# Kernel optimization log

Measured on AMD Instinct MI355X. Metric: run time of the kernel, lower is better.

## Reference

```python
import jax, jax.numpy as jnp
import numpy as np

B, S, H = 4, 1024, 1024
NH = 16
D = H // NH  # attention_head_size = 64
L = 9        # num_labels
MAXREL = 5
B_PERSON = 1
I_PERSON = 2
LN_EPS = 1e-5


def setup_inputs() -> dict:
    key = jax.random.key(0)
    ks = jax.random.split(key, 16)
    lin = lambda k, i, o: 0.02 * jax.random.normal(k, (i, o), jnp.float32)
    return {
        "sequence_output": jax.random.normal(ks[0], (B, S, H), jnp.float32),
        "Wq": lin(ks[1], H, H), "bq": jnp.zeros((H,), jnp.float32),
        "Wk": lin(ks[2], H, H), "bk": jnp.zeros((H,), jnp.float32),
        "Wv": lin(ks[3], H, H), "bv": jnp.zeros((H,), jnp.float32),
        "Wo": lin(ks[4], H, H), "bo": jnp.zeros((H,), jnp.float32),
        "ln_g": jnp.ones((H,), jnp.float32), "ln_b": jnp.zeros((H,), jnp.float32),
        "Ws": lin(ks[5], H, L), "bs": jnp.zeros((L,), jnp.float32),
        "entity_bias": 0.1 * jax.random.normal(ks[6], (L,), jnp.float32),
        "rel_pos_emb": jax.random.normal(ks[7], (2 * MAXREL + 1, D), jnp.float32),  # declared but unused in forward math, matching the torch module
    }


def reference(sequence_output, Wq, bq, Wk, bk, Wv, bv, Wo, bo, ln_g, ln_b, Ws, bs, entity_bias, rel_pos_emb):
    x = sequence_output  # [B,S,H]
    b, s, _ = x.shape

    def heads(t):  # [B,S,H] -> [B,NH,S,D]
        return t.reshape(b, s, NH, D).transpose(0, 2, 1, 3)

    q = heads(x @ Wq + bq)
    k = heads(x @ Wk + bk)
    v = heads(x @ Wv + bv)

    scores = jnp.einsum('bhqd,bhkd->bhqk', q, k)  # [B,NH,S,S]

    r = jnp.arange(s, dtype=jnp.float32)
    dist = jnp.abs(r[:, None] - r[None, :])                 # |i-j|, [S,S]
    pos_bias = jnp.exp(-0.1 * jnp.clip(dist, 0.0, float(MAXREL)))
    # torch order: (scores + pos_bias) / sqrt(D) + distance_mask
    scores = (scores + pos_bias) / np.sqrt(D) + (-0.1) * dist

    probs = jax.nn.softmax(scores, axis=-1)  # dropout is identity in eval
    ctx = jnp.einsum('bhqk,bhkd->bhqd', probs, v)
    ctx = ctx.transpose(0, 2, 1, 3).reshape(b, s, H)

    y = x + (ctx @ Wo + bo)  # residual
    mu = y.mean(-1, keepdims=True)
    var = y.var(-1, keepdims=True)
    yn = (y - mu) / jnp.sqrt(var + LN_EPS) * ln_g + ln_b

    span_logits = yn @ Ws + bs  # [B,S,L]
    # entity-bias loop: if argmax(span_logits[i,j-1]) == B-PERSON, add entity_bias[I-PERSON] twice to final[i,j,I-PERSON]
    prev_is_b = (jnp.argmax(span_logits[:, :-1, :], axis=-1) == B_PERSON).astype(span_logits.dtype)  # [B,S-1]
    final_logits = span_logits.at[:, 1:, I_PERSON].add(2.0 * entity_bias[I_PERSON] * prev_is_b)
    return final_logits
```

## Files before the change

### kernel.cpp

```cpp
#include <hip/hip_runtime.h>
#include <hip/hip_bf16.h>
#include <math.h>

typedef unsigned short ush;
typedef __attribute__((ext_vector_type(8))) _Float16 fragh;
typedef __attribute__((ext_vector_type(4))) _Float16 half4;
typedef __attribute__((ext_vector_type(4))) float f32x4;

#define S_   1024
#define H_   1024
#define NH_  16
#define D_   64
#define L_   9
#define MB_  (1048576ull)

__device__ __forceinline__ void load_lds16(const ush* g, const ush* l) {
  __builtin_amdgcn_global_load_lds(
      (const __attribute__((address_space(1))) void*)g,
      (__attribute__((address_space(3))) void*)l, 16, 0, 0);
}

__global__ __launch_bounds__(256) void prep(
    const float* __restrict__ x,
    const float* W0, const float* W1, const float* W2, const float* W3,
    const float* __restrict__ Ws,
    ush* __restrict__ xh, ush* T0, ush* T1, ush* T2, ush* T3,
    float* __restrict__ WsT) {
  __shared__ __align__(16) float Ls[64][68];
  const int bid = blockIdx.x;
  const int tid = threadIdx.x;

  if (bid < 2048) {
    const size_t i = ((size_t)bid * 256 + tid) * 8;
    float4 a = *(const float4*)&x[i];
    float4 b = *(const float4*)&x[i + 4];
    fragh v;
    v[0] = (_Float16)a.x; v[1] = (_Float16)a.y;
    v[2] = (_Float16)a.z; v[3] = (_Float16)a.w;
    v[4] = (_Float16)b.x; v[5] = (_Float16)b.y;
    v[6] = (_Float16)b.z; v[7] = (_Float16)b.w;
    *(fragh*)&xh[i] = v;
    return;
  }
  if (bid >= 3072) {
    for (int idx = tid; idx < 1024 * 9; idx += 256) {
      const int r = idx / 9, c = idx - r * 9;
      WsT[c * 1024 + r] = Ws[idx];
    }
    return;
  }
  const int flat = bid - 2048;
  const int wz = flat >> 8, wy = (flat >> 4) & 15, wx = flat & 15;
  const float* W = (wz == 0) ? W0 : (wz == 1) ? W1 : (wz == 2) ? W2 : W3;
  ush* Th = (wz == 0) ? T0 : (wz == 1) ? T1 : (wz == 2) ? T2 : T3;
  const int n0 = wx * 64, k0 = wy * 64;
#pragma unroll
  for (int it = 0; it < 4; it++) {
    int f = tid + 256 * it;
    int row = f >> 4, nc = (f & 15) * 4;
    *(float4*)&Ls[row][nc] = *(const float4*)&W[(size_t)(k0 + row) * 1024 + n0 + nc];
  }
  __syncthreads();
#pragma unroll
  for (int it = 0; it < 2; it++) {
    int f = tid + 256 * it;
    int nrow = f >> 3, kc = (f & 7) * 8;
    fragh v;
#pragma unroll
    for (int u = 0; u < 8; u++) v[u] = (_Float16)Ls[kc + u][nrow];
    *(fragh*)&Th[(size_t)(n0 + nrow) * 1024 + k0 + kc] = v;
  }
}

__global__ __launch_bounds__(256) void gemm_qkv(
    const ush* __restrict__ xh,
    const ush* __restrict__ Bq, const ush* __restrict__ Bk,
    const ush* __restrict__ Bv,
    const float* __restrict__ bq, const float* __restrict__ bk,
    const float* __restrict__ bv,
    ush* __restrict__ qh, ush* __restrict__ kh, ush* __restrict__ vT) {
  __shared__ __align__(16) ush As[2][128][32];
  __shared__ __align__(16) ush Bs[2][128][32];
  const int tid = threadIdx.x, lane = tid & 63, wave = tid >> 6;
  const int l15 = lane & 15, quad = lane >> 4;
  const int m0 = blockIdx.y * 128, n0 = blockIdx.x * 128;
  const int z = blockIdx.z;
  const ush* Bg = (z == 0) ? Bq : (z == 1) ? Bk : Bv;
  const float* bias = (z == 0) ? bq : (z == 1) ? bk : bv;
  ush* outp = (z == 0) ? qh : (z == 1) ? kh : vT;

  const int wm = (wave >> 1) * 64, wn = (wave & 1) * 64;

  f32x4 acc[4][4];
#pragma unroll
  for (int i = 0; i < 4; i++)
#pragma unroll
    for (int j = 0; j < 4; j++) acc[i][j] = (f32x4){0.f, 0.f, 0.f, 0.f};

  auto stage = [&](int bi, int k0) {
#pragma unroll
    for (int jj = 0; jj < 2; jj++) {
      const int call = wave * 2 + jj;
      const int c = call * 64 + lane;
      const int r = c >> 2, ch = c & 3;
      load_lds16(xh + (size_t)(m0 + r) * 1024 + k0 + ch * 8,
                 &As[bi][0][0] + (size_t)call * 512);
    }
#pragma unroll
    for (int jj = 0; jj < 2; jj++) {
      const int call = wave * 2 + jj;
      const int c = call * 64 + lane;
      const int r = c >> 2, ch = c & 3;
      load_lds16(Bg + (size_t)(n0 + r) * 1024 + k0 + ch * 8,
                 &Bs[bi][0][0] + (size_t)call * 512);
    }
  };

  auto compute = [&](int cur) {
    fragh a[4];
#pragma unroll
    for (int s = 0; s < 4; s++)
      a[s] = *(const fragh*)&As[cur][wm + s * 16 + l15][quad * 8];
#pragma unroll
    for (int t = 0; t < 4; t++) {
      fragh bt = *(const fragh*)&Bs[cur][wn + t * 16 + l15][quad * 8];
#pragma unroll
      for (int mi = 0; mi < 4; mi++)
        acc[mi][t] = __builtin_amdgcn_mfma_f32_16x16x32_f16(
            a[mi], bt, acc[mi][t], 0, 0, 0);
    }
  };

  stage(0, 0);
#pragma unroll 1
  for (int t = 0; t < 31; ++t) {
    const int cur = t & 1;
    stage(cur ^ 1, (t + 1) << 5);
    __builtin_amdgcn_sched_barrier(0);
    asm volatile("s_waitcnt vmcnt(4)" ::: "memory");
    __builtin_amdgcn_sched_barrier(0);
    __builtin_amdgcn_s_barrier();
    compute(cur);
    __builtin_amdgcn_s_barrier();
  }
  __builtin_amdgcn_sched_barrier(0);
  asm volatile("s_waitcnt vmcnt(0)" ::: "memory");
  __builtin_amdgcn_sched_barrier(0);
  __builtin_amdgcn_s_barrier();
  compute(1);

#pragma unroll
  for (int mi = 0; mi < 4; mi++) {
    const int rbase = m0 + wm + mi * 16 + quad * 4;
    const int bb = rbase >> 10, ss = rbase & 1023;
#pragma unroll
    for (int ni = 0; ni < 4; ni++) {
      const int col = n0 + wn + ni * 16 + l15;
      const float bv_ = bias[col];
      const int hidx = col >> 6, d = col & 63;
      if (z == 2) {
        half4 p4;
        p4[0] = (_Float16)(acc[mi][ni][0] + bv_);
        p4[1] = (_Float16)(acc[mi][ni][1] + bv_);
        p4[2] = (_Float16)(acc[mi][ni][2] + bv_);
        p4[3] = (_Float16)(acc[mi][ni][3] + bv_);
        *(half4*)&outp[((size_t)(bb * NH_ + hidx) * D_ + d) * S_ + ss] = p4;
      } else {
#pragma unroll
        for (int r = 0; r < 4; r++) {
          const size_t o =
              ((size_t)(bb * NH_ + hidx) * S_ + (ss + r)) * D_ + d;
          *(_Float16*)&outp[o] = (_Float16)(acc[mi][ni][r] + bv_);
        }
      }
    }
  }
}

__global__ __launch_bounds__(256) void gemm_o(
    const ush* __restrict__ ctxh, const ush* __restrict__ Bo,
    const float* __restrict__ bo, const float* __restrict__ resid,
    ush* __restrict__ yh) {
  __shared__ __align__(16) ush As[2][128][32];
  __shared__ __align__(16) ush Bs[2][64][32];
  const int tid = threadIdx.x, lane = tid & 63, wave = tid >> 6;
  const int l15 = lane & 15, quad = lane >> 4;
  const int m0 = blockIdx.y * 128, n0 = blockIdx.x * 64;
  const int wm = (wave >> 1) * 64, wn = (wave & 1) * 32;

  f32x4 acc[4][2];
#pragma unroll
  for (int i = 0; i < 4; i++)
#pragma unroll
    for (int j = 0; j < 2; j++) acc[i][j] = (f32x4){0.f, 0.f, 0.f, 0.f};

  auto stage = [&](int bi, int k0) {
#pragma unroll
    for (int jj = 0; jj < 2; jj++) {
      const int call = wave * 2 + jj;
      const int c = call * 64 + lane;
      const int r = c >> 2, ch = c & 3;
      load_lds16(ctxh + (size_t)(m0 + r) * 1024 + k0 + ch * 8,
                 &As[bi][0][0] + (size_t)call * 512);
    }
    {
      const int c = wave * 64 + lane;
      const int r = c >> 2, ch = c & 3;
      load_lds16(Bo + (size_t)(n0 + r) * 1024 + k0 + ch * 8,
                 &Bs[bi][0][0] + (size_t)wave * 512);
    }
  };

  auto compute = [&](int cur) {
    fragh a[4], b[2];
#pragma unroll
    for (int s = 0; s < 4; s++)
      a[s] = *(const fragh*)&As[cur][wm + s * 16 + l15][quad * 8];
#pragma unroll
    for (int t = 0; t < 2; t++)
      b[t] = *(const fragh*)&Bs[cur][wn + t * 16 + l15][quad * 8];
#pragma unroll
    for (int mi = 0; mi < 4; mi++)
#pragma unroll
      for (int ni = 0; ni < 2; ni++)
        acc[mi][ni] = __builtin_amdgcn_mfma_f32_16x16x32_f16(
            a[mi], b[ni], acc[mi][ni], 0, 0, 0);
  };

  stage(0, 0);
#pragma unroll 1
  for (int t = 0; t < 31; ++t) {
    const int cur = t & 1;
    stage(cur ^ 1, (t + 1) << 5);
    __builtin_amdgcn_sched_barrier(0);
    asm volatile("s_waitcnt vmcnt(3)" ::: "memory");
    __builtin_amdgcn_sched_barrier(0);
    __builtin_amdgcn_s_barrier();
    compute(cur);
    __builtin_amdgcn_s_barrier();
  }
  __builtin_amdgcn_sched_barrier(0);
  asm volatile("s_waitcnt vmcnt(0)" ::: "memory");
  __builtin_amdgcn_sched_barrier(0);
  __builtin_amdgcn_s_barrier();
  compute(1);

#pragma unroll
  for (int mi = 0; mi < 4; mi++) {
    const int rbase = m0 + wm + mi * 16 + quad * 4;
#pragma unroll
    for (int ni = 0; ni < 2; ni++) {
      const int col = n0 + wn + ni * 16 + l15;
      const float bv_ = bo[col];
#pragma unroll
      for (int r = 0; r < 4; r++) {
        const int m = rbase + r;
        const float val =
            acc[mi][ni][r] + bv_ + resid[(size_t)m * 1024 + col];
        *(_Float16*)&yh[(size_t)m * 1024 + col] = (_Float16)val;
      }
    }
  }
}

__global__ __launch_bounds__(256) void attn2(
    const ush* __restrict__ qh, const ush* __restrict__ kh,
    const ush* __restrict__ vT, ush* __restrict__ ch) {
  __shared__ __align__(16) ush Kh[64][72];
  __shared__ __align__(16) ush VTs[64][72];
  __shared__ __align__(16) ush Pst[64][72];
  __shared__ float LUT[256];
  const int tid = threadIdx.x;
  const int lane = tid & 63, wave = tid >> 6;
  const int l15 = lane & 15, quad = lane >> 4;
  const int w16 = wave * 16;
  const int bh = blockIdx.y;
  const int b = bh >> 4, h = bh & 15;
  const int q0 = blockIdx.x * 64;

  const float K1 = 0.18033688011112042f;
  const float K2 = 0.14426950408889634f;
  {
    const float dd = (float)tid;
    LUT[tid] = __expf(-0.1f * fminf(dd, 5.0f)) * K1 - dd * K2
             - 2.8853900817779268f;
  }

  const size_t qrow = ((size_t)bh * S_ + q0 + w16 + l15) * D_;
  fragh a_h[2];
  a_h[0] = *(const fragh*)&qh[qrow + quad * 8];
  a_h[1] = *(const fragh*)&qh[qrow + 32 + quad * 8];

  f32x4 o[4];
  float lrow[4];
#pragma unroll
  for (int i = 0; i < 4; i++) {
    o[i] = (f32x4){0.f, 0.f, 0.f, 0.f};
    lrow[i] = 0.f;
  }

  const size_t kbase = (size_t)bh * S_ * D_;
  const size_t vbase = (size_t)bh * D_ * S_;

  const int jlo = (q0 > 128) ? q0 - 128 : 0;
  const int jend = (q0 + 192 < S_) ? q0 + 192 : S_;

  for (int j0 = jlo; j0 < jend; j0 += 64) {
    __syncthreads();
#pragma unroll
    for (int it = 0; it < 2; it++) {
      const int flat = tid + 256 * it;
      const int row = flat >> 3, dc = (flat & 7) * 8;
      *(uint4*)&Kh[row][dc] =
          *(const uint4*)&kh[kbase + (size_t)(j0 + row) * D_ + dc];
      *(uint4*)&VTs[row][dc] =
          *(const uint4*)&vT[vbase + (size_t)row * S_ + j0 + dc];
    }
    __syncthreads();

    f32x4 c4[4];
#pragma unroll
    for (int nt = 0; nt < 4; nt++) c4[nt] = (f32x4){0.f, 0.f, 0.f, 0.f};
    __builtin_amdgcn_s_setprio(1);
#pragma unroll
    for (int kk = 0; kk < 2; kk++) {
#pragma unroll
      for (int nt = 0; nt < 4; nt++) {
        fragh bh_ = *(const fragh*)&Kh[nt * 16 + l15][kk * 32 + quad * 8];
        c4[nt] = __builtin_amdgcn_mfma_f32_16x16x32_f16(a_h[kk], bh_, c4[nt], 0, 0, 0);
      }
    }
    __builtin_amdgcn_s_setprio(0);

    const int ib = q0 + w16 + quad * 4 - j0 - l15;
#pragma unroll
    for (int r = 0; r < 4; r++) {
#pragma unroll
      for (int nt = 0; nt < 4; nt++) {
        int di = ib + r - nt * 16;
        di = (di < 0) ? -di : di;
        const float sv = exp2f(fmaf(c4[nt][r], K1, LUT[di]));
        lrow[r] += sv;
        *(_Float16*)&Pst[w16 + quad * 4 + r][nt * 16 + l15] = (_Float16)sv;
      }
    }

    fragh pa[2];
    pa[0] = *(const fragh*)&Pst[w16 + l15][quad * 8];
    pa[1] = *(const fragh*)&Pst[w16 + l15][32 + quad * 8];
    __builtin_amdgcn_s_setprio(1);
#pragma unroll
    for (int dt = 0; dt < 4; dt++) {
      fragh vb0 = *(const fragh*)&VTs[dt * 16 + l15][quad * 8];
      fragh vb1 = *(const fragh*)&VTs[dt * 16 + l15][32 + quad * 8];
      o[dt] = __builtin_amdgcn_mfma_f32_16x16x32_f16(pa[0], vb0, o[dt], 0, 0, 0);
      o[dt] = __builtin_amdgcn_mfma_f32_16x16x32_f16(pa[1], vb1, o[dt], 0, 0, 0);
    }
    __builtin_amdgcn_s_setprio(0);
  }

#pragma unroll
  for (int r = 0; r < 4; r++) {
#pragma unroll
    for (int off = 1; off < 16; off <<= 1) lrow[r] += __shfl_xor(lrow[r], off);
    const float inv = 1.0f / lrow[r];
    const size_t rowp =
        ((size_t)(b * S_ + q0 + w16 + quad * 4 + r)) * H_ + h * 64;
#pragma unroll
    for (int dt = 0; dt < 4; dt++)
      *(_Float16*)&ch[rowp + dt * 16 + l15] = (_Float16)(o[dt][r] * inv);
  }
}

__global__ __launch_bounds__(256) void ln_span(
    const ush* __restrict__ yh, const float* __restrict__ g,
    const float* __restrict__ bta, const float* __restrict__ WsT,
    const float* __restrict__ bs, float* __restrict__ logits) {
  const int tid = threadIdx.x, lane = tid & 63, wave = tid >> 6;
  const int row = blockIdx.x * 4 + wave;
  const int h0 = lane * 16;
  const ush* yr = yh + (size_t)row * 1024 + h0;

  fragh v0 = *(const fragh*)yr;
  fragh v1 = *(const fragh*)(yr + 8);
  float v[16];
#pragma unroll
  for (int u = 0; u < 8; u++) { v[u] = (float)v0[u]; v[8 + u] = (float)v1[u]; }

  float s = 0.f, s2 = 0.f;
#pragma unroll
  for (int u = 0; u < 16; u++) { s += v[u]; s2 += v[u] * v[u]; }
#pragma unroll
  for (int off = 32; off; off >>= 1) {
    s += __shfl_xor(s, off);
    s2 += __shfl_xor(s2, off);
  }
  const float mu = s * (1.0f / 1024.0f);
  const float var = s2 * (1.0f / 1024.0f) - mu * mu;
  const float inv = rsqrtf(var + 1e-5f);

  float yn[16];
#pragma unroll
  for (int i = 0; i < 4; i++) {
    float4 gg = *(const float4*)&g[h0 + i * 4];
    float4 bb = *(const float4*)&bta[h0 + i * 4];
    yn[i * 4 + 0] = (v[i * 4 + 0] - mu) * inv * gg.x + bb.x;
    yn[i * 4 + 1] = (v[i * 4 + 1] - mu) * inv * gg.y + bb.y;
    yn[i * 4 + 2] = (v[i * 4 + 2] - mu) * inv * gg.z + bb.z;
    yn[i * 4 + 3] = (v[i * 4 + 3] - mu) * inv * gg.w + bb.w;
  }

  float lg[9];
#pragma unroll
  for (int l = 0; l < 9; l++) {
    float acc = 0.f;
#pragma unroll
    for (int i = 0; i < 4; i++) {
      float4 w4 = *(const float4*)&WsT[l * 1024 + h0 + i * 4];
      acc += yn[i * 4 + 0] * w4.x + yn[i * 4 + 1] * w4.y +
             yn[i * 4 + 2] * w4.z + yn[i * 4 + 3] * w4.w;
    }
    lg[l] = acc;
  }
#pragma unroll
  for (int l = 0; l < 9; l++) {
#pragma unroll
    for (int off = 32; off; off >>= 1) lg[l] += __shfl_xor(lg[l], off);
  }
  if (lane == 0) {
#pragma unroll
    for (int l = 0; l < 9; l++)
      logits[(size_t)row * 9 + l] = lg[l] + bs[l];
  }
}

__global__ __launch_bounds__(256) void final_kernel(
    const float* __restrict__ logits, const float* __restrict__ eb,
    float* __restrict__ out) {
  const int m = blockIdx.x * 256 + threadIdx.x;
  const int i = m & 1023;
  float cur[9];
#pragma unroll
  for (int l = 0; l < 9; l++) cur[l] = logits[(size_t)m * 9 + l];
  if (i > 0) {
    const float* prev = logits + (size_t)(m - 1) * 9;
    int am = 0;
    float best = prev[0];
#pragma unroll
    for (int l = 1; l < 9; l++) {
      float pv = prev[l];
      if (pv > best) { best = pv; am = l; }
    }
    if (am == 1) cur[2] += 2.0f * eb[2];
  }
#pragma unroll
  for (int l = 0; l < 9; l++) out[(size_t)m * 9 + l] = cur[l];
}

extern "C" void kernel_launch(void* const* d_in, const int* in_sizes, int n_in,
                              void* d_out, int out_size, void* d_ws, size_t ws_size,
                              hipStream_t stream) {
  const float* x    = (const float*)d_in[0];
  const float* Wq   = (const float*)d_in[1];
  const float* bq   = (const float*)d_in[2];
  const float* Wk   = (const float*)d_in[3];
  const float* bk   = (const float*)d_in[4];
  const float* Wv   = (const float*)d_in[5];
  const float* bv   = (const float*)d_in[6];
  const float* Wo   = (const float*)d_in[7];
  const float* bo   = (const float*)d_in[8];
  const float* ln_g = (const float*)d_in[9];
  const float* ln_b = (const float*)d_in[10];
  const float* Ws   = (const float*)d_in[11];
  const float* bs   = (const float*)d_in[12];
  const float* eb   = (const float*)d_in[13];
  float* out = (float*)d_out;
  char* W8 = (char*)d_ws;

  ush* WoT  = (ush*)(W8 + 0 * MB_);
  ush* WqT  = (ush*)(W8 + 2 * MB_);
  ush* WkT  = (ush*)(W8 + 4 * MB_);
  ush* WvT  = (ush*)(W8 + 6 * MB_);
  ush* xh   = (ush*)(W8 + 8 * MB_);
  ush* qh   = (ush*)(W8 + 16 * MB_);
  ush* kh   = (ush*)(W8 + 24 * MB_);
  ush* vT   = (ush*)(W8 + 32 * MB_);
  ush* ctxh = (ush*)(W8 + 40 * MB_);
  ush* yh   = (ush*)(W8 + 48 * MB_);
  float* lg_ws = (float*)(W8 + 56 * MB_);
  float* WsT   = (float*)(W8 + 60 * MB_);

  prep<<<3073, 256, 0, stream>>>(
      x, Wq, Wk, Wv, Wo, Ws, xh, WqT, WkT, WvT, WoT, WsT);

  gemm_qkv<<<dim3(8, 32, 3), 256, 0, stream>>>(
      xh, WqT, WkT, WvT, bq, bk, bv, qh, kh, vT);
  attn2<<<dim3(16, 64), 256, 0, stream>>>(qh, kh, vT, ctxh);
  gemm_o<<<dim3(16, 32), 256, 0, stream>>>(ctxh, WoT, bo, x, yh);
  ln_span<<<1024, 256, 0, stream>>>(yh, ln_g, ln_b, WsT, bs, lg_ws);
  final_kernel<<<16, 256, 0, stream>>>(lg_ws, eb, out);
}
```

Baseline: 204.2 us.

## Double K-step depth in gemm_o and register-prefetch K/V tiles in attention

gemm_o now stages two 32-wide K slabs per pipeline step, so it covers 64 columns of K per barrier pair and runs half as many loop iterations. The attention kernel prefetches the next K/V tile into registers while the current tile is being computed, instead of loading global memory synchronously before each compute phase. It also adds an occupancy hint to launch_bounds. The aim is to cut barrier and load-latency stalls, at the cost of doubling LDS use in gemm_o and raising register pressure in attn2.

```diff
diff --git a/kernel.cpp b/kernel.cpp
--- a/kernel.cpp
+++ b/kernel.cpp
@@ -181,8 +181,8 @@
     const ush* __restrict__ ctxh, const ush* __restrict__ Bo,
     const float* __restrict__ bo, const float* __restrict__ resid,
     ush* __restrict__ yh) {
-  __shared__ __align__(16) ush As[2][128][32];
-  __shared__ __align__(16) ush Bs[2][64][32];
+  __shared__ __align__(16) ush As[2][2][128][32];
+  __shared__ __align__(16) ush Bs[2][2][64][32];
   const int tid = threadIdx.x, lane = tid & 63, wave = tid >> 6;
   const int l15 = lane & 15, quad = lane >> 4;
   const int m0 = blockIdx.y * 128, n0 = blockIdx.x * 64;
@@ -196,44 +196,50 @@
 
   auto stage = [&](int bi, int k0) {
 #pragma unroll
+    for (int jj = 0; jj < 4; jj++) {
+      const int slab = jj >> 1;
+      const int cw = wave * 2 + (jj & 1);
+      const int c = cw * 64 + lane;
+      const int r = c >> 2, ch = c & 3;
+      load_lds16(ctxh + (size_t)(m0 + r) * 1024 + k0 + slab * 32 + ch * 8,
+                 &As[bi][slab][0][0] + (size_t)cw * 512);
+    }
+#pragma unroll
     for (int jj = 0; jj < 2; jj++) {
-      const int call = wave * 2 + jj;
-      const int c = call * 64 + lane;
-      const int r = c >> 2, ch = c & 3;
-      load_lds16(ctxh + (size_t)(m0 + r) * 1024 + k0 + ch * 8,
-                 &As[bi][0][0] + (size_t)call * 512);
-    }
-    {
+      const int slab = jj;
       const int c = wave * 64 + lane;
       const int r = c >> 2, ch = c & 3;
-      load_lds16(Bo + (size_t)(n0 + r) * 1024 + k0 + ch * 8,
-                 &Bs[bi][0][0] + (size_t)wave * 512);
+      load_lds16(Bo + (size_t)(n0 + r) * 1024 + k0 + slab * 32 + ch * 8,
+                 &Bs[bi][slab][0][0] + (size_t)wave * 512);
     }
   };
 
-  auto compute = [&](int cur) {
-    fragh a[4], b[2];
-#pragma unroll
-    for (int s = 0; s < 4; s++)
-      a[s] = *(const fragh*)&As[cur][wm + s * 16 + l15][quad * 8];
-#pragma unroll
-    for (int t = 0; t < 2; t++)
-      b[t] = *(const fragh*)&Bs[cur][wn + t * 16 + l15][quad * 8];
-#pragma unroll
-    for (int mi = 0; mi < 4; mi++)
-#pragma unroll
-      for (int ni = 0; ni < 2; ni++)
-        acc[mi][ni] = __builtin_amdgcn_mfma_f32_16x16x32_f16(
-            a[mi], b[ni], acc[mi][ni], 0, 0, 0);
+  auto compute = [&](int bi) {
+#pragma unroll
+    for (int slab = 0; slab < 2; slab++) {
+      fragh a[4], b[2];
+#pragma unroll
+      for (int s = 0; s < 4; s++)
+        a[s] = *(const fragh*)&As[bi][slab][wm + s * 16 + l15][quad * 8];
+#pragma unroll
+      for (int t = 0; t < 2; t++)
+        b[t] = *(const fragh*)&Bs[bi][slab][wn + t * 16 + l15][quad * 8];
+#pragma unroll
+      for (int mi = 0; mi < 4; mi++)
+#pragma unroll
+        for (int ni = 0; ni < 2; ni++)
+          acc[mi][ni] = __builtin_amdgcn_mfma_f32_16x16x32_f16(
+              a[mi], b[ni], acc[mi][ni], 0, 0, 0);
+    }
   };
 
   stage(0, 0);
 #pragma unroll 1
-  for (int t = 0; t < 31; ++t) {
+  for (int t = 0; t < 15; ++t) {
     const int cur = t & 1;
-    stage(cur ^ 1, (t + 1) << 5);
+    stage(cur ^ 1, (t + 1) << 6);
     __builtin_amdgcn_sched_barrier(0);
-    asm volatile("s_waitcnt vmcnt(3)" ::: "memory");
+    asm volatile("s_waitcnt vmcnt(6)" ::: "memory");
     __builtin_amdgcn_sched_barrier(0);
     __builtin_amdgcn_s_barrier();
     compute(cur);
@@ -263,7 +269,7 @@
   }
 }
 
-__global__ __launch_bounds__(256) void attn2(
+__global__ __launch_bounds__(256, 4) void attn2(
     const ush* __restrict__ qh, const ush* __restrict__ kh,
     const ush* __restrict__ vT, ush* __restrict__ ch) {
   __shared__ __align__(16) ush Kh[64][72];
@@ -305,16 +311,29 @@
   const int jlo = (q0 > 128) ? q0 - 128 : 0;
   const int jend = (q0 + 192 < S_) ? q0 + 192 : S_;
 
+  const int row0 = tid >> 3, dc0 = (tid & 7) * 8;
+  const int row1 = (tid + 256) >> 3, dc1 = (tid & 7) * 8;
+
+  uint4 kA0, kA1, vA0, vA1;
+  uint4 kB0 = {0, 0, 0, 0}, kB1 = {0, 0, 0, 0};
+  uint4 vB0 = {0, 0, 0, 0}, vB1 = {0, 0, 0, 0};
+  kA0 = *(const uint4*)&kh[kbase + (size_t)(jlo + row0) * D_ + dc0];
+  kA1 = *(const uint4*)&kh[kbase + (size_t)(jlo + row1) * D_ + dc1];
+  vA0 = *(const uint4*)&vT[vbase + (size_t)row0 * S_ + jlo + dc0];
+  vA1 = *(const uint4*)&vT[vbase + (size_t)row1 * S_ + jlo + dc1];
+
   for (int j0 = jlo; j0 < jend; j0 += 64) {
     __syncthreads();
-#pragma unroll
-    for (int it = 0; it < 2; it++) {
-      const int flat = tid + 256 * it;
-      const int row = flat >> 3, dc = (flat & 7) * 8;
-      *(uint4*)&Kh[row][dc] =
-          *(const uint4*)&kh[kbase + (size_t)(j0 + row) * D_ + dc];
-      *(uint4*)&VTs[row][dc] =
-          *(const uint4*)&vT[vbase + (size_t)row * S_ + j0 + dc];
+    *(uint4*)&Kh[row0][dc0] = kA0;
+    *(uint4*)&Kh[row1][dc1] = kA1;
+    *(uint4*)&VTs[row0][dc0] = vA0;
+    *(uint4*)&VTs[row1][dc1] = vA1;
+    const int jn = j0 + 64;
+    if (jn < jend) {
+      kB0 = *(const uint4*)&kh[kbase + (size_t)(jn + row0) * D_ + dc0];
+      kB1 = *(const uint4*)&kh[kbase + (size_t)(jn + row1) * D_ + dc1];
+      vB0 = *(const uint4*)&vT[vbase + (size_t)row0 * S_ + jn + dc0];
+      vB1 = *(const uint4*)&vT[vbase + (size_t)row1 * S_ + jn + dc1];
     }
     __syncthreads();
 
@@ -357,6 +376,8 @@
       o[dt] = __builtin_amdgcn_mfma_f32_16x16x32_f16(pa[1], vb1, o[dt], 0, 0, 0);
     }
     __builtin_amdgcn_s_setprio(0);
+
+    kA0 = kB0; kA1 = kB1; vA0 = vB0; vA1 = vB1;
   }
 
 #pragma unroll
```

Measured after the change: 196.7 us (median of 3 runs). -3.7%, faster.
